# Performance work log

Measured on AMD Instinct MI355X. Metric: run time of the kernel, lower is better.

## Reference

```python
import jax, jax.numpy as jnp
import numpy as np

N = 100000
E = 1600000
IN_F = 128
OUT_F = 128
EPS = 1e-12


def setup_inputs() -> dict:
    key = jax.random.key(0)
    k1, k2, k3, k4, k5, k6 = jax.random.split(key, 6)
    x = jax.random.normal(k1, (N, IN_F), dtype=jnp.float32)
    rows = jnp.sort(jax.random.randint(k2, (E,), 0, N, dtype=jnp.int32))
    cols = jax.random.randint(k3, (E,), 0, N, dtype=jnp.int32)
    vals = jax.random.uniform(k4, (E,), dtype=jnp.float32)
    # nn.Linear(2*in_features, out_features): W is [out, 2*in], b is [out]
    bound = 1.0 / np.sqrt(2 * IN_F)
    W = jax.random.uniform(k5, (OUT_F, 2 * IN_F), dtype=jnp.float32, minval=-bound, maxval=bound)
    b = jax.random.uniform(k6, (OUT_F,), dtype=jnp.float32, minval=-bound, maxval=bound)
    return {"x": x, "rows": rows, "cols": cols, "vals": vals, "W": W, "b": b}


def reference(x, rows, cols, vals, W, b):
    # spmm(adj, x): gather source-node features, scale by edge weight,
    # segment-sum into destination rows.
    gathered = vals[:, None] * x[cols]                      # [E, in]
    neighbor = jax.ops.segment_sum(gathered, rows, num_segments=N)  # [N, in]
    combined = jnp.concatenate([x, neighbor], axis=1)       # [N, 2*in]
    out = combined @ W.T + b                                # [N, out]
    # F.normalize(out, p=2, dim=1): divide by max(||row||_2, eps)
    norm = jnp.sqrt(jnp.sum(out * out, axis=1, keepdims=True))
    return out / jnp.maximum(norm, EPS)
```

## Files before the change

### kernel.cpp

```cpp
#include <hip/hip_runtime.h>
#include <hip/hip_bf16.h>


typedef __bf16 bf16x8_t __attribute__((ext_vector_type(8)));
typedef float f32x4_t __attribute__((ext_vector_type(4)));

__device__ __forceinline__ unsigned int f32_to_bf16(float f) {
    unsigned int u = __float_as_uint(f);
    unsigned int r = u + 0x7fffu + ((u >> 16) & 1u);
    return r >> 16;
}
__device__ __forceinline__ unsigned int pack2(float a, float b) {
    return f32_to_bf16(a) | (f32_to_bf16(b) << 16);
}
__device__ __forceinline__ float bflo(unsigned int p) { return __uint_as_float(p << 16); }
__device__ __forceinline__ float bfhi(unsigned int p) { return __uint_as_float(p & 0xffff0000u); }

__global__ void rowptr_kernel(const int* __restrict__ rows, int* __restrict__ row_ptr,
                              int Nn, int Ee) {
    int n = blockIdx.x * blockDim.x + threadIdx.x;
    if (n > Nn) return;
    int lo = 0, hi = Ee;
    while (lo < hi) {
        int mid = (lo + hi) >> 1;
        if (rows[mid] < n) lo = mid + 1; else hi = mid;
    }
    row_ptr[n] = lo;
}

__global__ void wcast_kernel(const float* __restrict__ W, uint4* __restrict__ Wf) {
    int i = blockIdx.x * blockDim.x + threadIdx.x;
    int lane = i & 63, ks = (i >> 6) & 7, t = i >> 9;
    int row = t * 16 + (lane & 15);
    int col = ks * 32 + (lane >> 4) * 8;
    const float* p = W + (size_t)row * 256 + col;
    uint4 o;
    o.x = pack2(p[0], p[1]); o.y = pack2(p[2], p[3]);
    o.z = pack2(p[4], p[5]); o.w = pack2(p[6], p[7]);
    Wf[i] = o;
}

__global__ void xcast_kernel(const float* __restrict__ x, uint2* __restrict__ xb,
                             int total ) {
    int i = blockIdx.x * blockDim.x + threadIdx.x;
    if (i >= total) return;
    float4 f = ((const float4*)x)[i];
    uint2 o; o.x = pack2(f.x, f.y); o.y = pack2(f.z, f.w);
    xb[i] = o;
}

__global__ __launch_bounds__(64) void agg_kernel(const int* __restrict__ row_ptr,
                                                 const int* __restrict__ cols,
                                                 const float* __restrict__ vals,
                                                 const uint2* __restrict__ xb,
                                                 uint2* __restrict__ nb) {
    int n = blockIdx.x;
    int lane = threadIdx.x;
    int h = lane >> 5;
    int l = lane & 31;
    int start = row_ptr[n], end = row_ptr[n + 1];
    float a0 = 0.f, a1 = 0.f, a2 = 0.f, a3 = 0.f;

    int c0 = 0, c1 = 0, c2 = 0, c3 = 0;
    float v0 = 0.f, v1 = 0.f, v2 = 0.f, v3 = 0.f;

#define LOADG(E, C0, C1, C2, C3, V0, V1, V2, V3)                                   \
    {                                                                              \
        int m0 = (E) + h, m1 = (E) + 2 + h, m2 = (E) + 4 + h, m3 = (E) + 6 + h;    \
        int q0 = min(m0, end - 1), q1 = min(m1, end - 1);                          \
        int q2 = min(m2, end - 1), q3 = min(m3, end - 1);                          \
        C0 = cols[q0]; C1 = cols[q1]; C2 = cols[q2]; C3 = cols[q3];                \
        V0 = (m0 < end) ? vals[q0] : 0.f; V1 = (m1 < end) ? vals[q1] : 0.f;        \
        V2 = (m2 < end) ? vals[q2] : 0.f; V3 = (m3 < end) ? vals[q3] : 0.f;        \
    }

    int e = start;
    if (e < end) LOADG(e, c0, c1, c2, c3, v0, v1, v2, v3);
    while (e < end) {
        int en = e + 8;
        int d0 = 0, d1 = 0, d2 = 0, d3 = 0;
        float w0 = 0.f, w1 = 0.f, w2 = 0.f, w3 = 0.f;
        if (en < end) LOADG(en, d0, d1, d2, d3, w0, w1, w2, w3);
        uint2 p0 = xb[(size_t)c0 * 32 + l];
        uint2 p1 = xb[(size_t)c1 * 32 + l];
        uint2 p2 = xb[(size_t)c2 * 32 + l];
        uint2 p3 = xb[(size_t)c3 * 32 + l];
        a0 += v0 * bflo(p0.x); a1 += v0 * bfhi(p0.x); a2 += v0 * bflo(p0.y); a3 += v0 * bfhi(p0.y);
        a0 += v1 * bflo(p1.x); a1 += v1 * bfhi(p1.x); a2 += v1 * bflo(p1.y); a3 += v1 * bfhi(p1.y);
        a0 += v2 * bflo(p2.x); a1 += v2 * bfhi(p2.x); a2 += v2 * bflo(p2.y); a3 += v2 * bfhi(p2.y);
        a0 += v3 * bflo(p3.x); a1 += v3 * bfhi(p3.x); a2 += v3 * bflo(p3.y); a3 += v3 * bfhi(p3.y);
        c0 = d0; c1 = d1; c2 = d2; c3 = d3;
        v0 = w0; v1 = w1; v2 = w2; v3 = w3;
        e = en;
    }
#undef LOADG

    a0 += __shfl_xor(a0, 32, 64);
    a1 += __shfl_xor(a1, 32, 64);
    a2 += __shfl_xor(a2, 32, 64);
    a3 += __shfl_xor(a3, 32, 64);

    if (h == 0) {
        uint2 o; o.x = pack2(a0, a1); o.y = pack2(a2, a3);
        nb[(size_t)n * 32 + l] = o;
    }
}

__global__ __launch_bounds__(256) void gemm_norm_kernel(
        const unsigned short* __restrict__ xb, const unsigned short* __restrict__ nb,
        const bf16x8_t* __restrict__ Wf, const float* __restrict__ b,
        float* __restrict__ out, int Nn) {
    int lane = threadIdx.x & 63;
    int wave = threadIdx.x >> 6;
    int m    = lane & 15;
    int quad = lane >> 4;
    int r0   = (blockIdx.x * 4 + wave) * 16;

    int arow = r0 + m;
    if (arow >= Nn) arow = Nn - 1;
    const bf16x8_t* Ax = (const bf16x8_t*)(xb + (size_t)arow * 128);
    const bf16x8_t* An = (const bf16x8_t*)(nb + (size_t)arow * 128);

    bf16x8_t a[8];
#pragma unroll
    for (int ks = 0; ks < 4; ++ks) a[ks]     = Ax[ks * 4 + quad];
#pragma unroll
    for (int ks = 0; ks < 4; ++ks) a[4 + ks] = An[ks * 4 + quad];

    f32x4_t acc[8];
#pragma unroll
    for (int t = 0; t < 8; ++t) acc[t] = (f32x4_t){0.f, 0.f, 0.f, 0.f};

#pragma unroll
    for (int t = 0; t < 8; ++t) {
#pragma unroll
        for (int ks = 0; ks < 8; ++ks) {
            acc[t] = __builtin_amdgcn_mfma_f32_16x16x32_bf16(
                a[ks], Wf[(t * 8 + ks) * 64 + lane], acc[t], 0, 0, 0);
        }
    }

    float bc[8];
#pragma unroll
    for (int t = 0; t < 8; ++t) bc[t] = b[t * 16 + m];

    float sq[4] = {0.f, 0.f, 0.f, 0.f};
#pragma unroll
    for (int t = 0; t < 8; ++t)
#pragma unroll
        for (int r = 0; r < 4; ++r) {
            float v = acc[t][r] + bc[t];
            sq[r] += v * v;
        }
#pragma unroll
    for (int off = 1; off <= 8; off <<= 1) {
#pragma unroll
        for (int r = 0; r < 4; ++r) sq[r] += __shfl_xor(sq[r], off, 64);
    }
    float scale[4];
#pragma unroll
    for (int r = 0; r < 4; ++r) scale[r] = 1.f / fmaxf(sqrtf(sq[r]), 1e-12f);

#pragma unroll
    for (int r = 0; r < 4; ++r) {
        int row = r0 + quad * 4 + r;
        if (row < Nn) {
            float* orow = out + (size_t)row * 128;
#pragma unroll
            for (int t = 0; t < 8; ++t) {
                float v = acc[t][r] + bc[t];
                orow[t * 16 + m] = v * scale[r];
            }
        }
    }
}

extern "C" void kernel_launch(void* const* d_in, const int* in_sizes, int n_in,
                              void* d_out, int out_size, void* d_ws, size_t ws_size,
                              hipStream_t stream) {
    const float* x    = (const float*)d_in[0];
    const int*   rows = (const int*)  d_in[1];
    const int*   cols = (const int*)  d_in[2];
    const float* vals = (const float*)d_in[3];
    const float* W    = (const float*)d_in[4];
    const float* b    = (const float*)d_in[5];
    float*       out  = (float*)d_out;

    const int Nn = in_sizes[0] / 128;
    const int Ee = in_sizes[1];

    char* ws = (char*)d_ws;
    int*   row_ptr = (int*)ws;
    uint4* Wf      = (uint4*)(ws + 448 * 1024);
    uint2* xb      = (uint2*)(ws + 640 * 1024);
    uint2* nb      = (uint2*)(ws + 640 * 1024 + (size_t)Nn * 256);

    rowptr_kernel<<<(Nn + 256) / 256, 256, 0, stream>>>(rows, row_ptr, Nn, Ee);
    wcast_kernel<<<16, 256, 0, stream>>>(W, Wf);
    xcast_kernel<<<(Nn * 32 + 255) / 256, 256, 0, stream>>>(x, xb, Nn * 32);
    agg_kernel<<<Nn, 64, 0, stream>>>(row_ptr, cols, vals, xb, nb);
    gemm_norm_kernel<<<(Nn + 63) / 64, 256, 0, stream>>>(
        (const unsigned short*)xb, (const unsigned short*)nb,
        (const bf16x8_t*)Wf, b, out, Nn);
}
```

Baseline: 210.0 us.

## Merge prep kernels, remap aggregation to 16 lanes per row, double GEMM rows per wave

```diff
diff --git a/kernel.cpp b/kernel.cpp
--- a/kernel.cpp
+++ b/kernel.cpp
@@ -4,6 +4,7 @@
 
 typedef __bf16 bf16x8_t __attribute__((ext_vector_type(8)));
 typedef float f32x4_t __attribute__((ext_vector_type(4)));
+typedef float f32x2_t __attribute__((ext_vector_type(2)));
 
 __device__ __forceinline__ unsigned int f32_to_bf16(float f) {
     unsigned int u = __float_as_uint(f);
@@ -16,97 +17,104 @@
 __device__ __forceinline__ float bflo(unsigned int p) { return __uint_as_float(p << 16); }
 __device__ __forceinline__ float bfhi(unsigned int p) { return __uint_as_float(p & 0xffff0000u); }
 
-__global__ void rowptr_kernel(const int* __restrict__ rows, int* __restrict__ row_ptr,
-                              int Nn, int Ee) {
-    int n = blockIdx.x * blockDim.x + threadIdx.x;
-    if (n > Nn) return;
-    int lo = 0, hi = Ee;
-    while (lo < hi) {
-        int mid = (lo + hi) >> 1;
-        if (rows[mid] < n) lo = mid + 1; else hi = mid;
-    }
-    row_ptr[n] = lo;
-}
-
-__global__ void wcast_kernel(const float* __restrict__ W, uint4* __restrict__ Wf) {
-    int i = blockIdx.x * blockDim.x + threadIdx.x;
-    int lane = i & 63, ks = (i >> 6) & 7, t = i >> 9;
-    int row = t * 16 + (lane & 15);
-    int col = ks * 32 + (lane >> 4) * 8;
-    const float* p = W + (size_t)row * 256 + col;
-    uint4 o;
-    o.x = pack2(p[0], p[1]); o.y = pack2(p[2], p[3]);
-    o.z = pack2(p[4], p[5]); o.w = pack2(p[6], p[7]);
-    Wf[i] = o;
-}
-
-__global__ void xcast_kernel(const float* __restrict__ x, uint2* __restrict__ xb,
-                             int total ) {
-    int i = blockIdx.x * blockDim.x + threadIdx.x;
-    if (i >= total) return;
-    float4 f = ((const float4*)x)[i];
-    uint2 o; o.x = pack2(f.x, f.y); o.y = pack2(f.z, f.w);
-    xb[i] = o;
-}
-
-__global__ __launch_bounds__(64) void agg_kernel(const int* __restrict__ row_ptr,
-                                                 const int* __restrict__ cols,
-                                                 const float* __restrict__ vals,
-                                                 const uint2* __restrict__ xb,
-                                                 uint2* __restrict__ nb) {
-    int n = blockIdx.x;
-    int lane = threadIdx.x;
-    int h = lane >> 5;
-    int l = lane & 31;
-    int start = row_ptr[n], end = row_ptr[n + 1];
-    float a0 = 0.f, a1 = 0.f, a2 = 0.f, a3 = 0.f;
-
-    int c0 = 0, c1 = 0, c2 = 0, c3 = 0;
-    float v0 = 0.f, v1 = 0.f, v2 = 0.f, v3 = 0.f;
-
-#define LOADG(E, C0, C1, C2, C3, V0, V1, V2, V3)                                   \
-    {                                                                              \
-        int m0 = (E) + h, m1 = (E) + 2 + h, m2 = (E) + 4 + h, m3 = (E) + 6 + h;    \
-        int q0 = min(m0, end - 1), q1 = min(m1, end - 1);                          \
-        int q2 = min(m2, end - 1), q3 = min(m3, end - 1);                          \
-        C0 = cols[q0]; C1 = cols[q1]; C2 = cols[q2]; C3 = cols[q3];                \
-        V0 = (m0 < end) ? vals[q0] : 0.f; V1 = (m1 < end) ? vals[q1] : 0.f;        \
-        V2 = (m2 < end) ? vals[q2] : 0.f; V3 = (m3 < end) ? vals[q3] : 0.f;        \
+__global__ void prep_kernel(const float* __restrict__ x, uint4* __restrict__ xb4,
+                            const int* __restrict__ rows, int* __restrict__ row_ptr,
+                            const float* __restrict__ W, uint4* __restrict__ Wf,
+                            int Nn, int Ee, int xcast_blks, int rowptr_blks) {
+    int blk = blockIdx.x;
+    if (blk < xcast_blks) {
+        int i = blk * 256 + threadIdx.x;
+        if (i < Nn * 16) {
+            const float4* xf = (const float4*)x;
+            float4 f0 = xf[(size_t)i * 2];
+            float4 f1 = xf[(size_t)i * 2 + 1];
+            uint4 o;
+            o.x = pack2(f0.x, f0.y); o.y = pack2(f0.z, f0.w);
+            o.z = pack2(f1.x, f1.y); o.w = pack2(f1.z, f1.w);
+            xb4[i] = o;
+        }
+    } else if (blk < xcast_blks + rowptr_blks) {
+        int n = (blk - xcast_blks) * 256 + threadIdx.x;
+        if (n <= Nn) {
+            int lo = 0, hi = Ee;
+            while (lo < hi) {
+                int mid = (lo + hi) >> 1;
+                if (rows[mid] < n) lo = mid + 1; else hi = mid;
+            }
+            row_ptr[n] = lo;
+        }
+    } else {
+        int i = (blk - xcast_blks - rowptr_blks) * 256 + threadIdx.x;
+        int lane = i & 63, ks = (i >> 6) & 7, t = i >> 9;
+        int row = t * 16 + (lane & 15);
+        int col = ks * 32 + (lane >> 4) * 8;
+        const float* p = W + (size_t)row * 256 + col;
+        uint4 o;
+        o.x = pack2(p[0], p[1]); o.y = pack2(p[2], p[3]);
+        o.z = pack2(p[4], p[5]); o.w = pack2(p[6], p[7]);
+        Wf[i] = o;
+    }
+}
+
+__global__ __launch_bounds__(256, 8) void agg_kernel(
+        const int* __restrict__ row_ptr, const int* __restrict__ cols,
+        const float* __restrict__ vals, const char* __restrict__ xb,
+        uint4* __restrict__ nb, int Nn) {
+    int lane = threadIdx.x & 63;
+    int wave = threadIdx.x >> 6;
+    int h = lane >> 4;
+    int l = lane & 15;
+    int n = (blockIdx.x * 4 + wave) * 4 + h;
+    bool valid = n < Nn;
+    int nn = valid ? n : Nn - 1;
+    int start = row_ptr[nn], end = row_ptr[nn + 1];
+    if (!valid) end = start;
+    unsigned loff = (unsigned)l << 4;
+
+    f32x2_t a0 = {0.f, 0.f}, a1 = {0.f, 0.f}, a2 = {0.f, 0.f}, a3 = {0.f, 0.f};
+
+#define EDGE(E, C, V)                                              \
+    {                                                              \
+        int q = max(min((E), end - 1), 0);                         \
+        C = cols[q];                                               \
+        V = ((E) < end) ? vals[q] : 0.f;                           \
+    }
+#define ACC(P, V)                                                  \
+    {                                                              \
+        f32x2_t vv = {(V), (V)};                                   \
+        f32x2_t t0 = {bflo((P).x), bfhi((P).x)};                   \
+        f32x2_t t1 = {bflo((P).y), bfhi((P).y)};                   \
+        f32x2_t t2 = {bflo((P).z), bfhi((P).z)};                   \
+        f32x2_t t3 = {bflo((P).w), bfhi((P).w)};                   \
+        a0 += vv * t0; a1 += vv * t1; a2 += vv * t2; a3 += vv * t3;\
     }
 
     int e = start;
-    if (e < end) LOADG(e, c0, c1, c2, c3, v0, v1, v2, v3);
+    int c0 = 0, c1 = 0; float v0 = 0.f, v1 = 0.f;
+    if (e < end) { EDGE(e, c0, v0); EDGE(e + 1, c1, v1); }
     while (e < end) {
-        int en = e + 8;
-        int d0 = 0, d1 = 0, d2 = 0, d3 = 0;
-        float w0 = 0.f, w1 = 0.f, w2 = 0.f, w3 = 0.f;
-        if (en < end) LOADG(en, d0, d1, d2, d3, w0, w1, w2, w3);
-        uint2 p0 = xb[(size_t)c0 * 32 + l];
-        uint2 p1 = xb[(size_t)c1 * 32 + l];
-        uint2 p2 = xb[(size_t)c2 * 32 + l];
-        uint2 p3 = xb[(size_t)c3 * 32 + l];
-        a0 += v0 * bflo(p0.x); a1 += v0 * bfhi(p0.x); a2 += v0 * bflo(p0.y); a3 += v0 * bfhi(p0.y);
-        a0 += v1 * bflo(p1.x); a1 += v1 * bfhi(p1.x); a2 += v1 * bflo(p1.y); a3 += v1 * bfhi(p1.y);
-        a0 += v2 * bflo(p2.x); a1 += v2 * bfhi(p2.x); a2 += v2 * bflo(p2.y); a3 += v2 * bfhi(p2.y);
-        a0 += v3 * bflo(p3.x); a1 += v3 * bfhi(p3.x); a2 += v3 * bflo(p3.y); a3 += v3 * bfhi(p3.y);
-        c0 = d0; c1 = d1; c2 = d2; c3 = d3;
-        v0 = w0; v1 = w1; v2 = w2; v3 = w3;
-        e = en;
-    }
-#undef LOADG
-
-    a0 += __shfl_xor(a0, 32, 64);
-    a1 += __shfl_xor(a1, 32, 64);
-    a2 += __shfl_xor(a2, 32, 64);
-    a3 += __shfl_xor(a3, 32, 64);
-
-    if (h == 0) {
-        uint2 o; o.x = pack2(a0, a1); o.y = pack2(a2, a3);
-        nb[(size_t)n * 32 + l] = o;
-    }
-}
-
-__global__ __launch_bounds__(256) void gemm_norm_kernel(
+        int e2 = e + 2;
+        int d0 = 0, d1 = 0; float w0 = 0.f, w1 = 0.f;
+        if (e2 < end) { EDGE(e2, d0, w0); EDGE(e2 + 1, d1, w1); }
+        uint4 p0 = *(const uint4*)(xb + (((unsigned)c0 << 8) | loff));
+        uint4 p1 = *(const uint4*)(xb + (((unsigned)c1 << 8) | loff));
+        ACC(p0, v0);
+        ACC(p1, v1);
+        c0 = d0; v0 = w0; c1 = d1; v1 = w1;
+        e = e2;
+    }
+#undef EDGE
+#undef ACC
+
+    if (valid) {
+        uint4 o;
+        o.x = pack2(a0.x, a0.y); o.y = pack2(a1.x, a1.y);
+        o.z = pack2(a2.x, a2.y); o.w = pack2(a3.x, a3.y);
+        nb[(size_t)n * 16 + l] = o;
+    }
+}
+
+__global__ __launch_bounds__(256, 3) void gemm_norm_kernel(
         const unsigned short* __restrict__ xb, const unsigned short* __restrict__ nb,
         const bf16x8_t* __restrict__ Wf, const float* __restrict__ b,
         float* __restrict__ out, int Nn) {
@@ -114,29 +122,38 @@
     int wave = threadIdx.x >> 6;
     int m    = lane & 15;
     int quad = lane >> 4;
-    int r0   = (blockIdx.x * 4 + wave) * 16;
-
-    int arow = r0 + m;
-    if (arow >= Nn) arow = Nn - 1;
-    const bf16x8_t* Ax = (const bf16x8_t*)(xb + (size_t)arow * 128);
-    const bf16x8_t* An = (const bf16x8_t*)(nb + (size_t)arow * 128);
-
-    bf16x8_t a[8];
-#pragma unroll
-    for (int ks = 0; ks < 4; ++ks) a[ks]     = Ax[ks * 4 + quad];
-#pragma unroll
-    for (int ks = 0; ks < 4; ++ks) a[4 + ks] = An[ks * 4 + quad];
-
-    f32x4_t acc[8];
-#pragma unroll
-    for (int t = 0; t < 8; ++t) acc[t] = (f32x4_t){0.f, 0.f, 0.f, 0.f};
-
+    int r0   = (blockIdx.x * 4 + wave) * 32;
+
+    int arow0 = min(r0 + m, Nn - 1);
+    int arow1 = min(r0 + 16 + m, Nn - 1);
+    const bf16x8_t* Ax0 = (const bf16x8_t*)(xb + (size_t)arow0 * 128);
+    const bf16x8_t* An0 = (const bf16x8_t*)(nb + (size_t)arow0 * 128);
+    const bf16x8_t* Ax1 = (const bf16x8_t*)(xb + (size_t)arow1 * 128);
+    const bf16x8_t* An1 = (const bf16x8_t*)(nb + (size_t)arow1 * 128);
+
+    bf16x8_t a0[8], a1[8];
+#pragma unroll
+    for (int ks = 0; ks < 4; ++ks) {
+        a0[ks]     = Ax0[ks * 4 + quad];
+        a0[4 + ks] = An0[ks * 4 + quad];
+        a1[ks]     = Ax1[ks * 4 + quad];
+        a1[4 + ks] = An1[ks * 4 + quad];
+    }
+
+    f32x4_t acc0[8], acc1[8];
 #pragma unroll
     for (int t = 0; t < 8; ++t) {
+        acc0[t] = (f32x4_t){0.f, 0.f, 0.f, 0.f};
+        acc1[t] = (f32x4_t){0.f, 0.f, 0.f, 0.f};
+    }
+
+#pragma unroll
+    for (int t = 0; t < 8; ++t) {
 #pragma unroll
         for (int ks = 0; ks < 8; ++ks) {
-            acc[t] = __builtin_amdgcn_mfma_f32_16x16x32_bf16(
-                a[ks], Wf[(t * 8 + ks) * 64 + lane], acc[t], 0, 0, 0);
+            bf16x8_t B = Wf[(t * 8 + ks) * 64 + lane];
+            acc0[t] = __builtin_amdgcn_mfma_f32_16x16x32_bf16(a0[ks], B, acc0[t], 0, 0, 0);
+            acc1[t] = __builtin_amdgcn_mfma_f32_16x16x32_bf16(a1[ks], B, acc1[t], 0, 0, 0);
         }
     }
 
@@ -144,33 +161,44 @@
 #pragma unroll
     for (int t = 0; t < 8; ++t) bc[t] = b[t * 16 + m];
 
-    float sq[4] = {0.f, 0.f, 0.f, 0.f};
+    float sq0[4] = {0.f, 0.f, 0.f, 0.f}, sq1[4] = {0.f, 0.f, 0.f, 0.f};
 #pragma unroll
     for (int t = 0; t < 8; ++t)
 #pragma unroll
         for (int r = 0; r < 4; ++r) {
-            float v = acc[t][r] + bc[t];
-            sq[r] += v * v;
+            float u0 = acc0[t][r] + bc[t];
+            float u1 = acc1[t][r] + bc[t];
+            sq0[r] += u0 * u0;
+            sq1[r] += u1 * u1;
         }
 #pragma unroll
     for (int off = 1; off <= 8; off <<= 1) {
 #pragma unroll
-        for (int r = 0; r < 4; ++r) sq[r] += __shfl_xor(sq[r], off, 64);
-    }
-    float scale[4];
-#pragma unroll
-    for (int r = 0; r < 4; ++r) scale[r] = 1.f / fmaxf(sqrtf(sq[r]), 1e-12f);
-
+        for (int r = 0; r < 4; ++r) {
+            sq0[r] += __shfl_xor(sq0[r], off, 64);
+            sq1[r] += __shfl_xor(sq1[r], off, 64);
+        }
+    }
+    float sc0[4], sc1[4];
 #pragma unroll
     for (int r = 0; r < 4; ++r) {
-        int row = r0 + quad * 4 + r;
-        if (row < Nn) {
-            float* orow = out + (size_t)row * 128;
-#pragma unroll
-            for (int t = 0; t < 8; ++t) {
-                float v = acc[t][r] + bc[t];
-                orow[t * 16 + m] = v * scale[r];
-            }
+        sc0[r] = 1.f / fmaxf(sqrtf(sq0[r]), 1e-12f);
+        sc1[r] = 1.f / fmaxf(sqrtf(sq1[r]), 1e-12f);
+    }
+
+#pragma unroll
+    for (int r = 0; r < 4; ++r) {
+        int row0 = r0 + quad * 4 + r;
+        int row1 = r0 + 16 + quad * 4 + r;
+        if (row0 < Nn) {
+            float* orow = out + (size_t)row0 * 128;
+#pragma unroll
+            for (int t = 0; t < 8; ++t) orow[t * 16 + m] = (acc0[t][r] + bc[t]) * sc0[r];
+        }
+        if (row1 < Nn) {
+            float* orow = out + (size_t)row1 * 128;
+#pragma unroll
+            for (int t = 0; t < 8; ++t) orow[t * 16 + m] = (acc1[t][r] + bc[t]) * sc1[r];
         }
     }
 }
@@ -189,17 +217,21 @@
     const int Nn = in_sizes[0] / 128;
     const int Ee = in_sizes[1];
 
-    char* ws = (char*)d_ws;
+    char*  ws      = (char*)d_ws;
     int*   row_ptr = (int*)ws;
     uint4* Wf      = (uint4*)(ws + 448 * 1024);
-    uint2* xb      = (uint2*)(ws + 640 * 1024);
-    uint2* nb      = (uint2*)(ws + 640 * 1024 + (size_t)Nn * 256);
-
-    rowptr_kernel<<<(Nn + 256) / 256, 256, 0, stream>>>(rows, row_ptr, Nn, Ee);
-    wcast_kernel<<<16, 256, 0, stream>>>(W, Wf);
-    xcast_kernel<<<(Nn * 32 + 255) / 256, 256, 0, stream>>>(x, xb, Nn * 32);
-    agg_kernel<<<Nn, 64, 0, stream>>>(row_ptr, cols, vals, xb, nb);
-    gemm_norm_kernel<<<(Nn + 63) / 64, 256, 0, stream>>>(
+    uint4* xb      = (uint4*)(ws + 640 * 1024);
+    uint4* nb      = (uint4*)(ws + 640 * 1024 + (size_t)Nn * 256);
+
+    const int xcast_blks  = (Nn * 16 + 255) / 256;
+    const int rowptr_blks = (Nn + 1 + 255) / 256;
+    const int wcast_blks  = 16;
+
+    prep_kernel<<<xcast_blks + rowptr_blks + wcast_blks, 256, 0, stream>>>(
+        x, xb, rows, row_ptr, W, Wf, Nn, Ee, xcast_blks, rowptr_blks);
+    agg_kernel<<<(Nn + 15) / 16, 256, 0, stream>>>(
+        row_ptr, cols, vals, (const char*)xb, nb, Nn);
+    gemm_norm_kernel<<<(Nn + 127) / 128, 256, 0, stream>>>(
         (const unsigned short*)xb, (const unsigned short*)nb,
         (const bf16x8_t*)Wf, b, out, Nn);
 }
```

Result: slower. 214.5 us (+2.1%).
